# Optimization experiments

Hardware: AMD Instinct MI355X
Metric: run time of the kernel (lower is better)

Reference implementation:

```python
import jax, jax.numpy as jnp
import numpy as np

FRAME = 160      # frame_size
K = 15           # frames_per_payload
ORDER = 12       # lpc_order
B = 4096
T = K * FRAME    # 2400


def setup_inputs() -> dict:
    key = jax.random.key(0)
    k1, k2 = jax.random.split(key)
    bits = jax.random.randint(k1, (B, K), 0, 2, dtype=jnp.int32)
    pcm = jax.random.uniform(k2, (B, T, 1), jnp.float32, minval=-1.0, maxval=1.0)
    alpha = jnp.float32(0.05)  # layer weight 'alpha' (alpha_init=0.05)
    return {"bits": bits, "pcm": pcm, "alpha": alpha}


def lpc_burg(x, order):
    """librosa.lpc (Burg's method), vectorized over all frames. x: (N, L)."""
    a = jnp.zeros((x.shape[0], order + 1), x.dtype).at[:, 0].set(1.0)
    f = x[:, 1:]          # forward prediction error
    b = x[:, :-1]         # backward prediction error
    den = jnp.sum(f * f + b * b, axis=-1)
    for i in range(order):  # small fixed-order unrolled loop
        reflect = -2.0 * jnp.sum(b * f, axis=-1) / den   # (N,)
        r = reflect[:, None]
        # a[j] <- a[j] + reflect * a[i+1-j] for j=0..i+1 (j=0 is a no-op since a[i+1]=0)
        a = a.at[:, : i + 2].set(a[:, : i + 2] + r * a[:, : i + 2][:, ::-1])
        f_tmp = f
        f = f + r * b
        b = b + r * f_tmp
        den = (1.0 - reflect * reflect) * den - b[:, -1] ** 2 - f[:, 0] ** 2
        f = f[:, 1:]
        b = b[:, :-1]
    return a  # (N, order+1), a[:,0]==1


def fir_filter(a, x):
    """scipy.signal.lfilter(a, [1.0], x): out[n] = sum_k a[k]*x[n-k], zero init."""
    L = x.shape[1]
    xpad = jnp.pad(x, ((0, 0), (ORDER, 0)))
    # X[:, n, k] = x[:, n-k]
    X = jnp.stack([xpad[:, ORDER - k: ORDER - k + L] for k in range(ORDER + 1)], axis=-1)
    return jnp.einsum('nlk,nk->nl', X, a)


def residual(pcm):
    # pcm: (B, T, 1) -> per-frame LPC residual, same shape
    frames = pcm[..., 0].reshape(-1, FRAME)                 # (B*K, FRAME)
    win = jnp.asarray(np.hanning(FRAME), dtype=pcm.dtype)   # Hann window for LPC analysis only
    a = lpc_burg(frames * win, ORDER)
    res = fir_filter(a, frames)                              # filter the RAW frame
    return res.reshape(pcm.shape[0], T, 1)


def reference(bits, pcm, alpha):
    res = residual(pcm)
    signs = 2.0 * bits.astype(pcm.dtype) - 1.0              # (B, K) in {-1,+1}
    chips = jnp.repeat(signs, FRAME, axis=1)[..., None]     # (B, T, 1)
    return pcm + alpha * res * chips
```

## Files before the change

### kernel.cpp

```cpp
#include <hip/hip_runtime.h>

#define FRAME 160
#define ORDER 12
#define NFRAMES (4096 * 15)
#define EPL 10
#define FPW 4
#define PADF 12
#define ROWL (PADF + FRAME)

template<int CTRL>
__device__ __forceinline__ float dppf(float v) {
    return __int_as_float(__builtin_amdgcn_update_dpp(
        0, __float_as_int(v), CTRL, 0xF, 0xF, true));
}

__device__ __forceinline__ float rowsum16(float v) {
    v += dppf<0xB1>(v);
    v += dppf<0x4E>(v);
    v += dppf<0x140>(v);
    v += dppf<0x141>(v);
    return v;
}

__global__ __launch_bounds__(256, 8) void ResidualEmbedding_70798240907390_kernel(
    const int* __restrict__ bits, const float* __restrict__ pcm,
    const float* __restrict__ alpha_p, float* __restrict__ out)
{
    const int tid  = threadIdx.x;
    const int wave = tid >> 6;
    const int lane = tid & 63;
    const int g    = lane >> 4;
    const int s    = lane & 15;
    const int wf0  = (blockIdx.x * 4 + wave) * FPW;
    const int f_id = wf0 + g;

    __shared__ float s_win[161];
    __shared__ float s_x[4][FPW * ROWL + 1];
    __shared__ float s_a[4][FPW][16];

    if (tid < 161) {
        float w = (tid < 160)
            ? 0.5f - 0.5f * __cosf(6.2831853071795864769f / 159.0f * (float)tid)
            : 0.0f;
        s_win[tid] = w;
    }
    if (lane < FPW * PADF) {
        int fr = lane / PADF, sl = lane % PADF;
        s_x[wave][fr * ROWL + sl] = 0.0f;
    }
    if (lane == 63) s_x[wave][FPW * ROWL] = 0.0f;
    {
        const float4* src = (const float4*)(pcm + (size_t)wf0 * FRAME);
#pragma unroll
        for (int it = 0; it < 3; ++it) {
            int id = lane + 64 * it;
            if (id < 160) {
                int fr = id / 40, ix = id % 40;
                *(float4*)&s_x[wave][fr * ROWL + PADF + 4 * ix] = src[fr * 40 + ix];
            }
        }
    }
    __syncthreads();

    const float* Xr = &s_x[wave][g * ROWL];
    const int p0 = s * EPL;

    const float ac = alpha_p[0] * (2.0f * (float)bits[f_id] - 1.0f);

    float F[EPL], B[EPL];
    {
        float pr[EPL + 1];
#pragma unroll
        for (int j = 0; j <= EPL; ++j)
            pr[j] = Xr[PADF + p0 + j] * s_win[p0 + j];
#pragma unroll
        for (int t = 0; t < EPL; ++t) { F[t] = pr[t + 1]; B[t] = pr[t]; }
    }
    B[EPL - 1] = (s == 15) ? 0.0f : B[EPL - 1];
    float dp0 = 0.0f, dp1 = 0.0f;
#pragma unroll
    for (int t = 0; t < EPL; ++t) {
        dp0 = fmaf(F[t], F[t], dp0);
        dp1 = fmaf(B[t], B[t], dp1);
    }
    float den = rowsum16(dp0 + dp1);

    float a  = (s == 0) ? 1.0f : 0.0f;
    float ar = (s == 1) ? 1.0f : 0.0f;
    float cpart = 0.0f, denScaled = 0.0f;

#pragma unroll
    for (int i = 0; i < ORDER; ++i) {
        float q0 = 0.0f, q1 = 0.0f;
#pragma unroll
        for (int t = 0; t < EPL; t += 2) {
            q0 = fmaf(F[t],     B[t],     q0);
            q1 = fmaf(F[t + 1], B[t + 1], q1);
        }
        float num = rowsum16(q0 + q1);
        if (i > 0) den = denScaled - rowsum16(cpart);
        float r = -2.0f * num * __builtin_amdgcn_rcpf(den);

        float a_new  = fmaf(r, ar, a);
        float ar_new = fmaf(r, a, ar);
        a  = a_new;
        ar = dppf<0x111>(ar_new);

#pragma unroll
        for (int t = 0; t < EPL; ++t) {
            float fo = F[t];
            F[t] = fmaf(r, B[t], fo);
            B[t] = fmaf(r, fo, B[t]);
        }

        const int pe = 158 - i;
        const int SL = pe / EPL, SS = pe % EPL;
        float fe = (s == 0)  ? F[0]  : 0.0f;
        float be = (s == SL) ? B[SS] : 0.0f;
        cpart = fmaf(fe, fe, be * be);
        denScaled = fmaf(-r * r, den, den);

        float up = dppf<0x101>(F[0]);
#pragma unroll
        for (int t = 0; t < EPL - 1; ++t) F[t] = F[t + 1];
        F[EPL - 1] = up;
        B[SS] = (s == SL) ? 0.0f : B[SS];
    }

    s_a[wave][g][s] = a;
    __syncthreads();
    float ak[ORDER + 1];
#pragma unroll
    for (int k = 0; k <= ORDER; ++k) ak[k] = s_a[wave][g][k];

    float Xw[EPL + ORDER];
    {
        const float2* Xp = (const float2*)(Xr + p0);
#pragma unroll
        for (int j = 0; j < (EPL + ORDER) / 2; ++j) {
            float2 v = Xp[j];
            Xw[2 * j] = v.x; Xw[2 * j + 1] = v.y;
        }
    }

    float2* og = (float2*)(out + (size_t)f_id * FRAME + p0);
#pragma unroll
    for (int t = 0; t < EPL; t += 2) {
        float acc0 = 0.0f, acc1 = 0.0f;
#pragma unroll
        for (int k = 0; k <= ORDER; ++k) {
            acc0 = fmaf(ak[k], Xw[ORDER + t - k],     acc0);
            acc1 = fmaf(ak[k], Xw[ORDER + t + 1 - k], acc1);
        }
        og[t / 2] = make_float2(fmaf(ac, acc0, Xw[ORDER + t]),
                                fmaf(ac, acc1, Xw[ORDER + t + 1]));
    }
}

extern "C" void kernel_launch(void* const* d_in, const int* in_sizes, int n_in,
                              void* d_out, int out_size, void* d_ws, size_t ws_size,
                              hipStream_t stream) {
    const int*   bits  = (const int*)d_in[0];
    const float* pcm   = (const float*)d_in[1];
    const float* alpha = (const float*)d_in[2];
    float*       out   = (float*)d_out;

    dim3 grid(NFRAMES / 16), block(256);
    hipLaunchKernelGGL(ResidualEmbedding_70798240907390_kernel, grid, block, 0, stream,
                       bits, pcm, alpha, out);
}
```

Measured before the change: 112.2 us.

## Process two frames per lane group using packed FP32 FMA

Each 16-lane group now handles two frames at once. The frames are interleaved in shared memory as float2 pairs, so the Burg recursion and the FIR filter can use packed v2f FMA (v_pk_fma_f32). This halves the grid and doubles the work per thread, aiming to double arithmetic throughput per instruction and amortize the DPP reductions. The cost is higher register pressure: the occupancy hint of 8 was dropped, and the DPP and rcp operations still run per component.

```diff
diff --git a/kernel.cpp b/kernel.cpp
--- a/kernel.cpp
+++ b/kernel.cpp
@@ -4,9 +4,14 @@
 #define ORDER 12
 #define NFRAMES (4096 * 15)
 #define EPL 10
-#define FPW 4
-#define PADF 12
-#define ROWL (PADF + FRAME)
+#define ROWP 174
+
+typedef float v2f __attribute__((ext_vector_type(2)));
+
+__device__ __forceinline__ v2f pkfma(v2f a, v2f b, v2f c) {
+    return __builtin_elementwise_fma(a, b, c);
+}
+__device__ __forceinline__ v2f splat2(float v) { v2f r; r.x = v; r.y = v; return r; }
 
 template<int CTRL>
 __device__ __forceinline__ float dppf(float v) {
@@ -21,8 +26,11 @@
     v += dppf<0x141>(v);
     return v;
 }
+__device__ __forceinline__ v2f rowsum16v(v2f v) {
+    v2f r; r.x = rowsum16(v.x); r.y = rowsum16(v.y); return r;
+}
 
-__global__ __launch_bounds__(256, 8) void ResidualEmbedding_70798240907390_kernel(
+__global__ __launch_bounds__(256) void ResidualEmbedding_70798240907390_kernel(
     const int* __restrict__ bits, const float* __restrict__ pcm,
     const float* __restrict__ alpha_p, float* __restrict__ out)
 {
@@ -31,12 +39,13 @@
     const int lane = tid & 63;
     const int g    = lane >> 4;
     const int s    = lane & 15;
-    const int wf0  = (blockIdx.x * 4 + wave) * FPW;
-    const int f_id = wf0 + g;
+    const int wf0  = (blockIdx.x * 4 + wave) * 8;
+    const int fA   = wf0 + 2 * g;
+    const int fB   = fA + 1;
 
+    __shared__ __align__(16) v2f s_x[4][4][ROWP];
     __shared__ float s_win[161];
-    __shared__ float s_x[4][FPW * ROWL + 1];
-    __shared__ float s_a[4][FPW][16];
+    __shared__ v2f  s_a[4][4][16];
 
     if (tid < 161) {
         float w = (tid < 160)
@@ -44,116 +53,123 @@
             : 0.0f;
         s_win[tid] = w;
     }
-    if (lane < FPW * PADF) {
-        int fr = lane / PADF, sl = lane % PADF;
-        s_x[wave][fr * ROWL + sl] = 0.0f;
-    }
-    if (lane == 63) s_x[wave][FPW * ROWL] = 0.0f;
+    if (lane < 48) { int gr = lane / 12, j = lane % 12; s_x[wave][gr][j] = splat2(0.f); }
+    if (lane < 4)  s_x[wave][lane][172] = splat2(0.f);
+
     {
-        const float4* src = (const float4*)(pcm + (size_t)wf0 * FRAME);
+        const float* pAg = pcm + (size_t)fA * FRAME;
+        const float* pBg = pcm + (size_t)fB * FRAME;
 #pragma unroll
-        for (int it = 0; it < 3; ++it) {
-            int id = lane + 64 * it;
-            if (id < 160) {
-                int fr = id / 40, ix = id % 40;
-                *(float4*)&s_x[wave][fr * ROWL + PADF + 4 * ix] = src[fr * 40 + ix];
+        for (int c = 0; c < 3; ++c) {
+            int p = 4 * s + 64 * c;
+            if (p < FRAME) {
+                float4 a4 = *(const float4*)(pAg + p);
+                float4 b4 = *(const float4*)(pBg + p);
+                float4* dst = (float4*)&s_x[wave][g][12 + p];
+                dst[0] = make_float4(a4.x, b4.x, a4.y, b4.y);
+                dst[1] = make_float4(a4.z, b4.z, a4.w, b4.w);
             }
         }
     }
     __syncthreads();
 
-    const float* Xr = &s_x[wave][g * ROWL];
+    const v2f* X = &s_x[wave][g][12];
     const int p0 = s * EPL;
 
-    const float ac = alpha_p[0] * (2.0f * (float)bits[f_id] - 1.0f);
-
-    float F[EPL], B[EPL];
+    v2f F[EPL], B[EPL];
     {
-        float pr[EPL + 1];
+        v2f pr[EPL + 1];
 #pragma unroll
         for (int j = 0; j <= EPL; ++j)
-            pr[j] = Xr[PADF + p0 + j] * s_win[p0 + j];
+            pr[j] = X[p0 + j] * s_win[p0 + j];
 #pragma unroll
         for (int t = 0; t < EPL; ++t) { F[t] = pr[t + 1]; B[t] = pr[t]; }
     }
-    B[EPL - 1] = (s == 15) ? 0.0f : B[EPL - 1];
-    float dp0 = 0.0f, dp1 = 0.0f;
+    if (s == 15) B[EPL - 1] = splat2(0.f);
+    v2f dpF = splat2(0.f), dpB = splat2(0.f);
 #pragma unroll
     for (int t = 0; t < EPL; ++t) {
-        dp0 = fmaf(F[t], F[t], dp0);
-        dp1 = fmaf(B[t], B[t], dp1);
+        dpF = pkfma(F[t], F[t], dpF);
+        dpB = pkfma(B[t], B[t], dpB);
     }
-    float den = rowsum16(dp0 + dp1);
+    v2f den = rowsum16v(dpF + dpB);
 
-    float a  = (s == 0) ? 1.0f : 0.0f;
-    float ar = (s == 1) ? 1.0f : 0.0f;
-    float cpart = 0.0f, denScaled = 0.0f;
+    v2f a  = (s == 0) ? splat2(1.f) : splat2(0.f);
+    v2f ar = (s == 1) ? splat2(1.f) : splat2(0.f);
+    v2f cp = splat2(0.f), dsc = splat2(0.f);
 
 #pragma unroll
     for (int i = 0; i < ORDER; ++i) {
-        float q0 = 0.0f, q1 = 0.0f;
+        v2f q0 = splat2(0.f), q1 = splat2(0.f);
 #pragma unroll
         for (int t = 0; t < EPL; t += 2) {
-            q0 = fmaf(F[t],     B[t],     q0);
-            q1 = fmaf(F[t + 1], B[t + 1], q1);
+            q0 = pkfma(F[t],     B[t],     q0);
+            q1 = pkfma(F[t + 1], B[t + 1], q1);
         }
-        float num = rowsum16(q0 + q1);
-        if (i > 0) den = denScaled - rowsum16(cpart);
-        float r = -2.0f * num * __builtin_amdgcn_rcpf(den);
+        v2f num = rowsum16v(q0 + q1);
+        if (i > 0) den = dsc - rowsum16v(cp);
+        v2f r;
+        r.x = -2.0f * num.x * __builtin_amdgcn_rcpf(den.x);
+        r.y = -2.0f * num.y * __builtin_amdgcn_rcpf(den.y);
 
-        float a_new  = fmaf(r, ar, a);
-        float ar_new = fmaf(r, a, ar);
-        a  = a_new;
-        ar = dppf<0x111>(ar_new);
+        v2f an  = pkfma(r, ar, a);
+        v2f arn = pkfma(r, a, ar);
+        a = an;
+        ar.x = dppf<0x111>(arn.x);
+        ar.y = dppf<0x111>(arn.y);
 
 #pragma unroll
         for (int t = 0; t < EPL; ++t) {
-            float fo = F[t];
-            F[t] = fmaf(r, B[t], fo);
-            B[t] = fmaf(r, fo, B[t]);
+            v2f fo = F[t];
+            F[t] = pkfma(r, B[t], fo);
+            B[t] = pkfma(r, fo, B[t]);
         }
 
         const int pe = 158 - i;
         const int SL = pe / EPL, SS = pe % EPL;
-        float fe = (s == 0)  ? F[0]  : 0.0f;
-        float be = (s == SL) ? B[SS] : 0.0f;
-        cpart = fmaf(fe, fe, be * be);
-        denScaled = fmaf(-r * r, den, den);
+        v2f fe = (s == 0)  ? F[0]  : splat2(0.f);
+        v2f be = (s == SL) ? B[SS] : splat2(0.f);
+        cp  = pkfma(fe, fe, be * be);
+        dsc = pkfma(-(r * r), den, den);
 
-        float up = dppf<0x101>(F[0]);
+        v2f up;
+        up.x = dppf<0x101>(F[0].x);
+        up.y = dppf<0x101>(F[0].y);
 #pragma unroll
         for (int t = 0; t < EPL - 1; ++t) F[t] = F[t + 1];
         F[EPL - 1] = up;
-        B[SS] = (s == SL) ? 0.0f : B[SS];
+        if (s == SL) B[SS] = splat2(0.f);
     }
 
     s_a[wave][g][s] = a;
     __syncthreads();
-    float ak[ORDER + 1];
+    v2f ak[ORDER + 1];
 #pragma unroll
     for (int k = 0; k <= ORDER; ++k) ak[k] = s_a[wave][g][k];
 
-    float Xw[EPL + ORDER];
-    {
-        const float2* Xp = (const float2*)(Xr + p0);
+    v2f Xw[EPL + ORDER];
 #pragma unroll
-        for (int j = 0; j < (EPL + ORDER) / 2; ++j) {
-            float2 v = Xp[j];
-            Xw[2 * j] = v.x; Xw[2 * j + 1] = v.y;
-        }
-    }
+    for (int j = 0; j < EPL + ORDER; ++j) Xw[j] = X[p0 - ORDER + j];
 
-    float2* og = (float2*)(out + (size_t)f_id * FRAME + p0);
+    const float alpha = alpha_p[0];
+    v2f ac;
+    ac.x = alpha * (2.0f * (float)bits[fA] - 1.0f);
+    ac.y = alpha * (2.0f * (float)bits[fB] - 1.0f);
+
+    float* oA = out + (size_t)fA * FRAME + p0;
+    float* oB = out + (size_t)fB * FRAME + p0;
 #pragma unroll
     for (int t = 0; t < EPL; t += 2) {
-        float acc0 = 0.0f, acc1 = 0.0f;
+        v2f acc0 = splat2(0.f), acc1 = splat2(0.f);
 #pragma unroll
         for (int k = 0; k <= ORDER; ++k) {
-            acc0 = fmaf(ak[k], Xw[ORDER + t - k],     acc0);
-            acc1 = fmaf(ak[k], Xw[ORDER + t + 1 - k], acc1);
+            acc0 = pkfma(ak[k], Xw[ORDER + t - k],     acc0);
+            acc1 = pkfma(ak[k], Xw[ORDER + t + 1 - k], acc1);
         }
-        og[t / 2] = make_float2(fmaf(ac, acc0, Xw[ORDER + t]),
-                                fmaf(ac, acc1, Xw[ORDER + t + 1]));
+        v2f r0 = pkfma(ac, acc0, Xw[ORDER + t]);
+        v2f r1 = pkfma(ac, acc1, Xw[ORDER + t + 1]);
+        *(float2*)(oA + t) = make_float2(r0.x, r1.x);
+        *(float2*)(oB + t) = make_float2(r0.y, r1.y);
     }
 }
 
@@ -165,7 +181,7 @@
     const float* alpha = (const float*)d_in[2];
     float*       out   = (float*)d_out;
 
-    dim3 grid(NFRAMES / 16), block(256);
+    dim3 grid(NFRAMES / 32), block(256);
     hipLaunchKernelGGL(ResidualEmbedding_70798240907390_kernel, grid, block, 0, stream,
                        bits, pcm, alpha, out);
 }
```

New measurement: 105.0 us. 6.4% less time.
